# Optimization experiments

Hardware: AMD Instinct MI355X
Metric: run time of the kernel (lower is better)

Reference implementation:

```python
import jax, jax.numpy as jnp
import numpy as np

B = 32768
DIM = 768          # emb dim
NA = 1024          # outer n_anchors
K = 8              # n_comp (= n_patches P in relays)
PD = 16            # patch_dim
RD = K * PD        # relay_dim = 128
L = 2              # n_layers (relays)
RA = 16            # anchors per patch inside RelayLayer
NPH = 3            # n_phases
TD = NPH * RA      # tri_dim = 48
H = 64             # pw_hidden
MAG_MIN, MAG_MAX = 0.1, 5.0


def _nrm(x, eps=1e-12):
    return x / jnp.maximum(jnp.linalg.norm(x, axis=-1, keepdims=True), eps)


def _ln(x, g, b, eps=1e-5):
    mu = jnp.mean(x, axis=-1, keepdims=True)
    var = jnp.mean(jnp.square(x - mu), axis=-1, keepdims=True)
    return (x - mu) * jax.lax.rsqrt(var + eps) * g + b


def setup_inputs() -> dict:
    key = jax.random.key(0)
    ks = jax.random.split(key, 16)
    xav = lambda k, shp, fan_in, fan_out: jax.random.normal(k, shp, jnp.float32) * np.sqrt(2.0 / (fan_in + fan_out))
    home = _nrm(jax.random.normal(ks[3], (L, K, RA, PD), jnp.float32))
    anchors = _nrm(home + 0.05 * jax.random.normal(ks[4], (L, K, RA, PD), jnp.float32))
    return {
        'emb': jax.random.normal(ks[0], (B, DIM), jnp.float32),
        'triangulation': jax.random.normal(ks[1], (B, NA), jnp.float32),
        'raw_magnitude': jax.random.uniform(ks[2], (B, 1), jnp.float32),
        'emb_w': xav(ks[5], (DIM, RD // 2), DIM, RD // 2), 'emb_b': jnp.zeros((RD // 2,), jnp.float32),
        'tri_w': xav(ks[6], (NA, RD // 4), NA, RD // 4), 'tri_b': jnp.zeros((RD // 4,), jnp.float32),
        'ctx_w': xav(ks[7], (RD // 2 + RD // 4 + 1, RD), RD // 2 + RD // 4 + 1, RD), 'ctx_b': jnp.zeros((RD,), jnp.float32),
        'home': home, 'anchors': anchors,
        'pw_w1': xav(ks[8], (L, K, TD, H), TD, H), 'pw_b1': jnp.zeros((L, K, H), jnp.float32),
        'pw_w2': xav(ks[9], (L, K, H, PD), H, PD), 'pw_b2': jnp.zeros((L, K, PD), jnp.float32),
        'pwn_g': jnp.ones((L, PD), jnp.float32), 'pwn_b': jnp.zeros((L, PD), jnp.float32),
        'gates': jnp.full((L, K), -3.0, jnp.float32),
        'norm_g': jnp.ones((L, RD), jnp.float32), 'norm_b': jnp.zeros((L, RD), jnp.float32),
        'head_w1': xav(ks[10], (K, PD, PD // 2), PD, PD // 2), 'head_b1': jnp.zeros((K, PD // 2), jnp.float32),
        'head_w2': xav(ks[11], (K, PD // 2, 1), PD // 2, 1), 'head_b2': jnp.zeros((K, 1), jnp.float32),
        'stats_bias': jnp.zeros((K,), jnp.float32),
    }


def _relay(x, home, anchors, w1, b1, w2, b2, pg, pb, gates, ng, nb):
    Bb = x.shape[0]
    patches = _ln(x, ng, nb).reshape(Bb, K, PD)          # [B,P,d]
    pn = _nrm(patches)
    h = _nrm(home)                                       # [P,A,d]
    c = _nrm(anchors)
    cosw = jnp.clip(jnp.sum(h * c, axis=-1), -1 + 1e-7, 1 - 1e-7)
    omega = jnp.arccos(cosw)[..., None]                  # [P,A,1]
    so = jnp.maximum(jnp.sin(omega), 1e-7)
    tris = []
    for t in (0.0, 1.0 / 3.0, 2.0 / 3.0):
        at = _nrm((jnp.sin((1.0 - t) * omega) * h + jnp.sin(t * omega) * c) / so)
        tris.append(1.0 - jnp.einsum('bpd,pad->bpa', pn, at))
    tri = jnp.concatenate(tris, axis=-1)                 # [B,P,3A]
    hh = jax.nn.gelu(jnp.einsum('bpt,pth->bph', tri, w1) + b1, approximate=False)
    pw = _ln(jnp.einsum('bph,phd->bpd', hh, w2) + b2, pg, pb)
    g = jax.nn.sigmoid(gates)[None, :, None]             # [1,P,1]
    return x + (g * pw + (1.0 - g) * patches).reshape(Bb, -1)


def reference(emb, triangulation, raw_magnitude, emb_w, emb_b, tri_w, tri_b, ctx_w, ctx_b,
              home, anchors, pw_w1, pw_b1, pw_w2, pw_b2, pwn_g, pwn_b, gates, norm_g, norm_b,
              head_w1, head_b1, head_w2, head_b2, stats_bias):
    ctx = jnp.concatenate([emb @ emb_w + emb_b, triangulation @ tri_w + tri_b, raw_magnitude], axis=-1)
    x = ctx @ ctx_w + ctx_b                              # [B, RD]
    for l in range(L):
        x = _relay(x, home[l], anchors[l], pw_w1[l], pw_b1[l], pw_w2[l], pw_b2[l],
                   pwn_g[l], pwn_b[l], gates[l], norm_g[l], norm_b[l])
    patches = x.reshape(-1, K, PD)
    h1 = jax.nn.gelu(jnp.einsum('bkd,kdh->bkh', patches, head_w1) + head_b1, approximate=False)
    mc_raw = (jnp.einsum('bkh,kho->bko', h1, head_w2) + head_b2)[..., 0]   # [B,K]
    mc = MAG_MIN + (MAG_MAX - MAG_MIN) * jax.nn.sigmoid(mc_raw + stats_bias)
    mag = jnp.repeat(mc, NA // K, axis=-1)               # [B, NA]
    return (mag, mc)
```

## Files before the change

kernel.cpp:

```cpp
#include <hip/hip_runtime.h>
#include <hip/hip_bf16.h>
#include <math.h>

#define BTOT 32768

typedef float f32x4 __attribute__((ext_vector_type(4)));
typedef __bf16 v8bf __attribute__((ext_vector_type(8)));

__device__ float g_x[BTOT * 128];
__device__ float g_M[2 * 8 * 16 * 64];
__device__ float g_b1p[2 * 8 * 64];
__device__ __align__(16) unsigned short g_wf[1792 * 128];
__device__ float g_beff[128];
__device__ float g_wr[128];

__device__ __forceinline__ float gelu_f(float v) {
    return 0.5f * v * (1.0f + erff(v * 0.70710678118654752f));
}

__device__ __forceinline__ unsigned short f2bf_rne(float x) {
    unsigned u = __float_as_uint(x);
    u += 0x7fffu + ((u >> 16) & 1u);
    return (unsigned short)(u >> 16);
}

#define GLOAD16(gp, lp)                                                        \
    __builtin_amdgcn_global_load_lds(                                          \
        (const __attribute__((address_space(1))) void*)(gp),                   \
        (__attribute__((address_space(3))) void*)(lp), 16, 0, 0)

__global__ __launch_bounds__(64) void k_pre(const float* __restrict__ home,
                                            const float* __restrict__ anchors,
                                            const float* __restrict__ pw_w1,
                                            const float* __restrict__ pw_b1) {
    __shared__ float s_AT[48 * 16];
    const int lp = blockIdx.x;
    const int tid = threadIdx.x;
    if (tid < 48) {
        const int t = tid >> 4, a = tid & 15;
        const float* hp = home + (lp * 16 + a) * 16;
        const float* cp = anchors + (lp * 16 + a) * 16;
        float h[16], c[16], nh = 0.f, nc = 0.f;
#pragma unroll
        for (int i = 0; i < 16; ++i) {
            h[i] = hp[i]; nh = fmaf(h[i], h[i], nh);
            c[i] = cp[i]; nc = fmaf(c[i], c[i], nc);
        }
        const float ih = 1.f / fmaxf(sqrtf(nh), 1e-12f);
        const float ic = 1.f / fmaxf(sqrtf(nc), 1e-12f);
        float cw = 0.f;
#pragma unroll
        for (int i = 0; i < 16; ++i) { h[i] *= ih; c[i] *= ic; cw = fmaf(h[i], c[i], cw); }
        cw = fminf(fmaxf(cw, -1.f + 1e-7f), 1.f - 1e-7f);
        const float om = acosf(cw);
        const float so = fmaxf(sinf(om), 1e-7f);
        const float tt = (float)t * (1.f / 3.f);
        const float s1 = sinf((1.f - tt) * om), s2 = sinf(tt * om);
        float v[16], nv = 0.f;
#pragma unroll
        for (int i = 0; i < 16; ++i) { v[i] = (s1 * h[i] + s2 * c[i]) / so; nv = fmaf(v[i], v[i], nv); }
        const float iv = 1.f / fmaxf(sqrtf(nv), 1e-12f);
#pragma unroll
        for (int i = 0; i < 16; ++i) s_AT[tid * 16 + i] = v[i] * iv;
    }
    __syncthreads();
    const int h = tid;
    const float* w1 = pw_w1 + lp * 48 * 64;
    float b = pw_b1[lp * 64 + h];
    float m[16];
#pragma unroll
    for (int d = 0; d < 16; ++d) m[d] = 0.f;
    for (int j = 0; j < 48; ++j) {
        const float w = w1[j * 64 + h];
        b += w;
#pragma unroll
        for (int d = 0; d < 16; ++d) m[d] = fmaf(s_AT[j * 16 + d], w, m[d]);
    }
    g_b1p[lp * 64 + h] = b;
#pragma unroll
    for (int d = 0; d < 16; ++d) g_M[(lp * 16 + d) * 64 + h] = m[d];
}

__global__ __launch_bounds__(256) void k_fold(const float* __restrict__ emb_w,
                                              const float* __restrict__ tri_w,
                                              const float* __restrict__ ctx_w,
                                              const float* __restrict__ ctx_b,
                                              const float* __restrict__ emb_b,
                                              const float* __restrict__ tri_b) {
    if (blockIdx.x == 56) {
        const int n = threadIdx.x;
        if (n < 128) {
            float b = ctx_b[n];
            for (int c = 0; c < 64; ++c) b = fmaf(emb_b[c], ctx_w[c * 128 + n], b);
            for (int c = 0; c < 32; ++c) b = fmaf(tri_b[c], ctx_w[(64 + c) * 128 + n], b);
            g_beff[n] = b;
            g_wr[n] = ctx_w[96 * 128 + n];
        }
        return;
    }
    __shared__ float sctx[97 * 128];
    for (int q = threadIdx.x; q < 3104; q += 256)
        *(float4*)&sctx[q * 4] = *(const float4*)&ctx_w[q * 4];
    __syncthreads();
    const int kt = blockIdx.x;
    const int kr = threadIdx.x >> 3;
    const int n0 = (threadIdx.x & 7) * 16;
    const int k = kt * 32 + kr;
    float acc[16];
#pragma unroll
    for (int j = 0; j < 16; ++j) acc[j] = 0.f;
    if (k < 768) {
        const float* wrow = emb_w + k * 64;
        for (int c = 0; c < 64; ++c) {
            const float a = wrow[c];
            const float* cx = &sctx[c * 128 + n0];
#pragma unroll
            for (int j = 0; j < 16; ++j) acc[j] = fmaf(a, cx[j], acc[j]);
        }
    } else {
        const float* wrow = tri_w + (k - 768) * 32;
        for (int c = 0; c < 32; ++c) {
            const float a = wrow[c];
            const float* cx = &sctx[(64 + c) * 128 + n0];
#pragma unroll
            for (int j = 0; j < 16; ++j) acc[j] = fmaf(a, cx[j], acc[j]);
        }
    }
    const int nt = threadIdx.x & 7;
    const int lanehi = (kr >> 3) << 4;
    const int j8 = kr & 7;
#pragma unroll
    for (int q = 0; q < 16; ++q) {
        const int lane = lanehi | q;
        g_wf[((kt * 8 + nt) * 64 + lane) * 8 + j8] = f2bf_rne(acc[q]);
    }
}

__global__ __launch_bounds__(256) void k_front_mfma(const float* __restrict__ emb,
                                                    const float* __restrict__ tri,
                                                    const float* __restrict__ rm) {
    __shared__ __align__(16) char lds[49152];
    const int tid = threadIdx.x;
    const int lane = tid & 63, w = tid >> 6;
    const int row0 = blockIdx.x * 64;
    const int arow = lane & 15, kgrp = lane >> 4;

    f32x4 acc[8];
#pragma unroll
    for (int nt = 0; nt < 8; ++nt) {
        f32x4 z = {0.f, 0.f, 0.f, 0.f};
        acc[nt] = z;
    }

    const float* embp = emb + (size_t)(row0 + w * 16 + arow) * 768 + kgrp * 8;
    const float* trip = tri + (size_t)(row0 + w * 16 + arow) * 1024 + kgrp * 8;

    float4 A0[4], A1[4], A2[4];

#define STAGE_B(kk, BUF) {                                                     \
        const int k2_ = (kk) < 27 ? (kk) : 27;                                 \
        const char* gB_ = (const char*)g_wf + (size_t)k2_ * 16384              \
                          + w * 4096 + lane * 16;                              \
        char* Bb_ = lds + (BUF) * 16384 + w * 4096;               \
        _Pragma("unroll")                                                      \
        for (int i = 0; i < 4; ++i) GLOAD16(gB_ + i * 1024, Bb_ + i * 1024);   \
    }

#define ALOAD(kk, S) {                                                         \
        const int k2_ = (kk) < 27 ? (kk) : 27;                                 \
        const float* ab_ = (k2_ < 12) ? (embp + k2_ * 64) : (trip + (k2_ - 12) * 64); \
        S[0] = *(const float4*)(ab_);                                          \
        S[1] = *(const float4*)(ab_ + 4);                                      \
        S[2] = *(const float4*)(ab_ + 32);                                     \
        S[3] = *(const float4*)(ab_ + 36);                                     \
    }

#define COMPUTE(BUF, S) {                                                      \
        const char* Br_ = lds + (BUF) * 16384 + lane * 16;                     \
        _Pragma("unroll")                                                      \
        for (int h = 0; h < 2; ++h) {                                          \
            const float4 f0_ = S[h * 2], f1_ = S[h * 2 + 1];                   \
            v8bf a_;                                                           \
            a_[0] = (__bf16)f0_.x; a_[1] = (__bf16)f0_.y;                      \
            a_[2] = (__bf16)f0_.z; a_[3] = (__bf16)f0_.w;                      \
            a_[4] = (__bf16)f1_.x; a_[5] = (__bf16)f1_.y;                      \
            a_[6] = (__bf16)f1_.z; a_[7] = (__bf16)f1_.w;                      \
            const char* bp_ = Br_ + h * 8192;                                  \
            _Pragma("unroll")                                                  \
            for (int nt = 0; nt < 8; ++nt) {                                   \
                const v8bf b_ = *(const v8bf*)(bp_ + nt * 1024);               \
                acc[nt] = __builtin_amdgcn_mfma_f32_16x16x32_bf16(a_, b_, acc[nt], 0, 0, 0); \
            }                                                                  \
        }                                                                      \
    }

#define BODY(kk, I0, I2, S0, S2) {                                             \
        STAGE_B((kk) + 2, I2);                                                 \
        ALOAD((kk) + 2, S2);                                                   \
        asm volatile("s_waitcnt vmcnt(16)" ::: "memory");                      \
        __builtin_amdgcn_s_barrier();                                          \
        COMPUTE(I0, S0);                                                       \
        __builtin_amdgcn_s_barrier();                                          \
    }

    STAGE_B(0, 0); ALOAD(0, A0);
    STAGE_B(1, 1); ALOAD(1, A1);

    for (int t = 0; t < 9; ++t) {
        const int k = t * 3;
        BODY(k,     0, 2, A0, A2);
        BODY(k + 1, 1, 0, A1, A0);
        BODY(k + 2, 2, 1, A2, A1);
    }
    BODY(27, 0, 2, A0, A2);
    asm volatile("s_waitcnt vmcnt(0)" ::: "memory");
#undef STAGE_B
#undef ALOAD
#undef COMPUTE
#undef BODY

    const int rowb = row0 + w * 16 + kgrp * 4;
    const f32x4 rv = *(const f32x4*)&rm[rowb];
#pragma unroll
    for (int nt = 0; nt < 8; ++nt) {
        const int col = nt * 16 + arow;
        const float be = g_beff[col];
        const float wv = g_wr[col];
#pragma unroll
        for (int rr = 0; rr < 4; ++rr) {
            g_x[(size_t)(rowb + rr) * 128 + col] = acc[nt][rr] + rv[rr] * wv + be;
        }
    }
}

__global__ __launch_bounds__(256) void k_relay(
    const float* __restrict__ pw_w2, const float* __restrict__ pw_b2,
    const float* __restrict__ pwn_g, const float* __restrict__ pwn_b,
    const float* __restrict__ gates, const float* __restrict__ norm_g,
    const float* __restrict__ norm_b, const float* __restrict__ head_w1,
    const float* __restrict__ head_b1, const float* __restrict__ head_w2,
    const float* __restrict__ head_b2, const float* __restrict__ stats_bias,
    float* __restrict__ out) {
    __shared__ __align__(16) float s_M[8 * 1028];
    __shared__ __align__(16) float s_w2[8 * 1028];
    __shared__ __align__(16) float s_b1p[8 * 68];
    __shared__ __align__(16) float s_hw1[8 * 132];
    __shared__ float s_hb1[64], s_hw2[64], s_hcb[8];
    __shared__ float s_mc[64 * 8];
    const int tid = threadIdx.x;
    const int pr = tid >> 3, p = tid & 7;
    const int rowA = blockIdx.x * 64 + pr * 2;

    {
        const int e = tid * 4, pp = e >> 7, rem = e & 127;
        *(float4*)&s_hw1[pp * 132 + rem] = *(const float4*)&head_w1[e];
    }
    if (tid < 64) { s_hb1[tid] = head_b1[tid]; s_hw2[tid] = head_w2[tid]; }
    if (tid < 8) s_hcb[tid] = head_b2[tid] + stats_bias[tid];

    float xA[16], xB[16];
    {
        const float* xp = g_x + (size_t)rowA * 128 + p * 16;
#pragma unroll
        for (int i = 0; i < 4; ++i) {
            *(float4*)&xA[i * 4] = *(const float4*)&xp[i * 4];
            *(float4*)&xB[i * 4] = *(const float4*)&xp[128 + i * 4];
        }
    }

    for (int l = 0; l < 2; ++l) {
        if (l) __syncthreads();
        for (int q = tid; q < 2048; q += 256) {
            const int e = q * 4, pp = e >> 10, rem = e & 1023;
            *(float4*)&s_M[pp * 1028 + rem] = *(const float4*)&g_M[l * 8192 + e];
            *(float4*)&s_w2[pp * 1028 + rem] = *(const float4*)&pw_w2[l * 8192 + e];
        }
        if (tid < 128) {
            const int e = tid * 4, pp = e >> 6, rem = e & 63;
            *(float4*)&s_b1p[pp * 68 + rem] = *(const float4*)&g_b1p[l * 512 + e];
        }
        __syncthreads();

        float sA = 0.f, qA = 0.f, sB = 0.f, qB = 0.f;
#pragma unroll
        for (int i = 0; i < 16; ++i) {
            sA += xA[i]; qA = fmaf(xA[i], xA[i], qA);
            sB += xB[i]; qB = fmaf(xB[i], xB[i], qB);
        }
#pragma unroll
        for (int m = 1; m < 8; m <<= 1) {
            sA += __shfl_xor(sA, m, 64); qA += __shfl_xor(qA, m, 64);
            sB += __shfl_xor(sB, m, 64); qB += __shfl_xor(qB, m, 64);
        }
        const float muA = sA * (1.f / 128.f);
        const float rsA = rsqrtf(fmaxf(qA * (1.f / 128.f) - muA * muA, 0.f) + 1e-5f);
        const float muB = sB * (1.f / 128.f);
        const float rsB = rsqrtf(fmaxf(qB * (1.f / 128.f) - muB * muB, 0.f) + 1e-5f);
        float paA[16], paB[16], nA = 0.f, nB = 0.f;
#pragma unroll
        for (int i = 0; i < 16; ++i) {
            const float gg = norm_g[l * 128 + p * 16 + i];
            const float bb = norm_b[l * 128 + p * 16 + i];
            const float vA = (xA[i] - muA) * rsA * gg + bb;
            const float vB = (xB[i] - muB) * rsB * gg + bb;
            paA[i] = vA; nA = fmaf(vA, vA, nA);
            paB[i] = vB; nB = fmaf(vB, vB, nB);
        }
        const float invA = 1.f / fmaxf(sqrtf(nA), 1e-12f);
        const float invB = 1.f / fmaxf(sqrtf(nB), 1e-12f);

        float pwA[16], pwB[16];
#pragma unroll
        for (int i = 0; i < 16; ++i) {
            const float b2 = pw_b2[(l * 8 + p) * 16 + i];
            pwA[i] = b2; pwB[i] = b2;
        }
        const float* Mp = &s_M[p * 1028];
        const float* W2p = &s_w2[p * 1028];
        const float* Bp = &s_b1p[p * 68];
        for (int h4 = 0; h4 < 16; ++h4) {
            float bq[4];
            *(float4*)bq = *(const float4*)&Bp[h4 * 4];
            float aA[4] = {0.f, 0.f, 0.f, 0.f};
            float aB[4] = {0.f, 0.f, 0.f, 0.f};
#pragma unroll
            for (int d = 0; d < 16; ++d) {
                float m4[4];
                *(float4*)m4 = *(const float4*)&Mp[d * 64 + h4 * 4];
#pragma unroll
                for (int j = 0; j < 4; ++j) {
                    aA[j] = fmaf(paA[d], m4[j], aA[j]);
                    aB[j] = fmaf(paB[d], m4[j], aB[j]);
                }
            }
#pragma unroll
            for (int j = 0; j < 4; ++j) {
                const float gA = gelu_f(bq[j] - invA * aA[j]);
                const float gB = gelu_f(bq[j] - invB * aB[j]);
                float w[16];
#pragma unroll
                for (int u = 0; u < 4; ++u)
                    *(float4*)&w[u * 4] = *(const float4*)&W2p[(h4 * 4 + j) * 16 + u * 4];
#pragma unroll
                for (int u = 0; u < 16; ++u) {
                    pwA[u] = fmaf(gA, w[u], pwA[u]);
                    pwB[u] = fmaf(gB, w[u], pwB[u]);
                }
            }
        }
        float s2A = 0.f, q2A = 0.f, s2B = 0.f, q2B = 0.f;
#pragma unroll
        for (int i = 0; i < 16; ++i) {
            s2A += pwA[i]; q2A = fmaf(pwA[i], pwA[i], q2A);
            s2B += pwB[i]; q2B = fmaf(pwB[i], pwB[i], q2B);
        }
        const float mu2A = s2A * (1.f / 16.f);
        const float rs2A = rsqrtf(fmaxf(q2A * (1.f / 16.f) - mu2A * mu2A, 0.f) + 1e-5f);
        const float mu2B = s2B * (1.f / 16.f);
        const float rs2B = rsqrtf(fmaxf(q2B * (1.f / 16.f) - mu2B * mu2B, 0.f) + 1e-5f);
        const float gate = 1.f / (1.f + expf(-gates[l * 8 + p]));
#pragma unroll
        for (int i = 0; i < 16; ++i) {
            const float pg = pwn_g[l * 16 + i], pb = pwn_b[l * 16 + i];
            const float vA = (pwA[i] - mu2A) * rs2A * pg + pb;
            const float vB = (pwB[i] - mu2B) * rs2B * pg + pb;
            xA[i] = xA[i] + gate * vA + (1.f - gate) * paA[i];
            xB[i] = xB[i] + gate * vB + (1.f - gate) * paB[i];
        }
    }

    float accmA = s_hcb[p], accmB = accmA;
#pragma unroll
    for (int j = 0; j < 8; ++j) {
        float aA = s_hb1[p * 8 + j], aB = aA;
#pragma unroll
        for (int d = 0; d < 16; ++d) {
            const float w = s_hw1[p * 132 + d * 8 + j];
            aA = fmaf(xA[d], w, aA);
            aB = fmaf(xB[d], w, aB);
        }
        const float w2h = s_hw2[p * 8 + j];
        accmA = fmaf(gelu_f(aA), w2h, accmA);
        accmB = fmaf(gelu_f(aB), w2h, accmB);
    }
    const float mcA = 0.1f + 4.9f / (1.f + expf(-accmA));
    const float mcB = 0.1f + 4.9f / (1.f + expf(-accmB));
    s_mc[(pr * 2) * 8 + p] = mcA;
    s_mc[(pr * 2 + 1) * 8 + p] = mcB;
    out[(size_t)33554432 + (size_t)rowA * 8 + p] = mcA;
    out[(size_t)33554432 + (size_t)(rowA + 1) * 8 + p] = mcB;
    __syncthreads();

    const size_t base = (size_t)blockIdx.x * 64 * 1024;
#pragma unroll
    for (int it = 0; it < 64; ++it) {
        const int idx = it * 256 + tid;
        const int rr = idx >> 8, c4 = idx & 255;
        const float v = s_mc[rr * 8 + (c4 >> 5)];
        const float4 vv = make_float4(v, v, v, v);
        *(float4*)&out[base + rr * 1024 + c4 * 4] = vv;
    }
}

extern "C" void kernel_launch(void* const* d_in, const int* in_sizes, int n_in,
                              void* d_out, int out_size, void* d_ws, size_t ws_size,
                              hipStream_t stream) {
    (void)in_sizes; (void)n_in; (void)d_ws; (void)ws_size; (void)out_size;
    const float* emb = (const float*)d_in[0];
    const float* tria = (const float*)d_in[1];
    const float* rm = (const float*)d_in[2];
    const float* emb_w = (const float*)d_in[3];
    const float* emb_b = (const float*)d_in[4];
    const float* tri_w = (const float*)d_in[5];
    const float* tri_b = (const float*)d_in[6];
    const float* ctx_w = (const float*)d_in[7];
    const float* ctx_b = (const float*)d_in[8];
    const float* home = (const float*)d_in[9];
    const float* anch = (const float*)d_in[10];
    const float* pw_w1 = (const float*)d_in[11];
    const float* pw_b1 = (const float*)d_in[12];
    const float* pw_w2 = (const float*)d_in[13];
    const float* pw_b2 = (const float*)d_in[14];
    const float* pwn_g = (const float*)d_in[15];
    const float* pwn_b = (const float*)d_in[16];
    const float* gates = (const float*)d_in[17];
    const float* norm_g = (const float*)d_in[18];
    const float* norm_b = (const float*)d_in[19];
    const float* hw1 = (const float*)d_in[20];
    const float* hb1 = (const float*)d_in[21];
    const float* hw2 = (const float*)d_in[22];
    const float* hb2 = (const float*)d_in[23];
    const float* sb = (const float*)d_in[24];
    float* out = (float*)d_out;

    k_pre<<<16, 64, 0, stream>>>(home, anch, pw_w1, pw_b1);
    k_fold<<<57, 256, 0, stream>>>(emb_w, tri_w, ctx_w, ctx_b, emb_b, tri_b);
    k_front_mfma<<<512, 256, 0, stream>>>(emb, tria, rm);
    k_relay<<<512, 256, 0, stream>>>(pw_w2, pw_b2, pwn_g, pwn_b, gates, norm_g, norm_b,
                                     hw1, hb1, hw2, hb2, sb, out);
}
```

Before: 178.4 us.

## Replace erf GELU with tanh approx, double-buffer front GEMM, 4 rows per relay thread

GELU now uses a sigmoid-based tanh approximation with fast exp and reciprocal instead of erff, and the sigmoids use fast reciprocal. The front MFMA kernel moves from a triple-buffered, waitcnt-tuned pipeline to a simpler double buffer with __syncthreads, which reduces LDS use. The relay kernel processes 4 rows per thread (128 rows per block, half the blocks) so each LDS weight load is reused across more rows. The GELU approximation changes numerics slightly, and the heavier register load per thread may reduce occupancy.

```diff
diff --git a/kernel.cpp b/kernel.cpp
--- a/kernel.cpp
+++ b/kernel.cpp
@@ -14,8 +14,21 @@
 __device__ float g_beff[128];
 __device__ float g_wr[128];
 
+__device__ __forceinline__ float fast_rcp(float x) {
+#if __has_builtin(__builtin_amdgcn_rcpf)
+    return __builtin_amdgcn_rcpf(x);
+#else
+    return 1.f / x;
+#endif
+}
+
 __device__ __forceinline__ float gelu_f(float v) {
-    return 0.5f * v * (1.0f + erff(v * 0.70710678118654752f));
+    const float p = v * fmaf(v * v, 0.0713548162f, 1.59576912f);
+    return v * fast_rcp(1.f + __expf(-p));
+}
+
+__device__ __forceinline__ float fast_sigmoid(float v) {
+    return fast_rcp(1.f + __expf(-v));
 }
 
 __device__ __forceinline__ unsigned short f2bf_rne(float x) {
@@ -139,7 +152,7 @@
 __global__ __launch_bounds__(256) void k_front_mfma(const float* __restrict__ emb,
                                                     const float* __restrict__ tri,
                                                     const float* __restrict__ rm) {
-    __shared__ __align__(16) char lds[49152];
+    __shared__ __align__(16) char lds[32768];
     const int tid = threadIdx.x;
     const int lane = tid & 63, w = tid >> 6;
     const int row0 = blockIdx.x * 64;
@@ -155,24 +168,23 @@
     const float* embp = emb + (size_t)(row0 + w * 16 + arow) * 768 + kgrp * 8;
     const float* trip = tri + (size_t)(row0 + w * 16 + arow) * 1024 + kgrp * 8;
 
-    float4 A0[4], A1[4], A2[4];
+    float4 A0[4], A1[4];
+
+#define ALOAD(kk, S) {                                                         \
+        const float* ab_ = ((kk) < 12) ? (embp + (kk) * 64)                    \
+                                       : (trip + ((kk) - 12) * 64);            \
+        S[0] = *(const float4*)(ab_);                                          \
+        S[1] = *(const float4*)(ab_ + 4);                                      \
+        S[2] = *(const float4*)(ab_ + 32);                                     \
+        S[3] = *(const float4*)(ab_ + 36);                                     \
+    }
 
 #define STAGE_B(kk, BUF) {                                                     \
-        const int k2_ = (kk) < 27 ? (kk) : 27;                                 \
-        const char* gB_ = (const char*)g_wf + (size_t)k2_ * 16384              \
+        const char* gB_ = (const char*)g_wf + (size_t)(kk) * 16384             \
                           + w * 4096 + lane * 16;                              \
         char* Bb_ = lds + (BUF) * 16384 + w * 4096;               \
         _Pragma("unroll")                                                      \
         for (int i = 0; i < 4; ++i) GLOAD16(gB_ + i * 1024, Bb_ + i * 1024);   \
-    }
-
-#define ALOAD(kk, S) {                                                         \
-        const int k2_ = (kk) < 27 ? (kk) : 27;                                 \
-        const float* ab_ = (k2_ < 12) ? (embp + k2_ * 64) : (trip + (k2_ - 12) * 64); \
-        S[0] = *(const float4*)(ab_);                                          \
-        S[1] = *(const float4*)(ab_ + 4);                                      \
-        S[2] = *(const float4*)(ab_ + 32);                                     \
-        S[3] = *(const float4*)(ab_ + 36);                                     \
     }
 
 #define COMPUTE(BUF, S) {                                                      \
@@ -194,30 +206,24 @@
         }                                                                      \
     }
 
-#define BODY(kk, I0, I2, S0, S2) {                                             \
-        STAGE_B((kk) + 2, I2);                                                 \
-        ALOAD((kk) + 2, S2);                                                   \
-        asm volatile("s_waitcnt vmcnt(16)" ::: "memory");                      \
-        __builtin_amdgcn_s_barrier();                                          \
-        COMPUTE(I0, S0);                                                       \
-        __builtin_amdgcn_s_barrier();                                          \
-    }
-
-    STAGE_B(0, 0); ALOAD(0, A0);
-    STAGE_B(1, 1); ALOAD(1, A1);
-
-    for (int t = 0; t < 9; ++t) {
-        const int k = t * 3;
-        BODY(k,     0, 2, A0, A2);
-        BODY(k + 1, 1, 0, A1, A0);
-        BODY(k + 2, 2, 1, A2, A1);
-    }
-    BODY(27, 0, 2, A0, A2);
-    asm volatile("s_waitcnt vmcnt(0)" ::: "memory");
+    ALOAD(0, A0);
+    STAGE_B(0, 0);
+    __syncthreads();
+    for (int t = 0; t < 14; ++t) {
+        ALOAD(2 * t + 1, A1);
+        STAGE_B(2 * t + 1, 1);
+        COMPUTE(0, A0);
+        __syncthreads();
+        if (t < 13) {
+            ALOAD(2 * t + 2, A0);
+            STAGE_B(2 * t + 2, 0);
+        }
+        COMPUTE(1, A1);
+        __syncthreads();
+    }
+#undef ALOAD
 #undef STAGE_B
-#undef ALOAD
 #undef COMPUTE
-#undef BODY
 
     const int rowb = row0 + w * 16 + kgrp * 4;
     const f32x4 rv = *(const f32x4*)&rm[rowb];
@@ -246,10 +252,10 @@
     __shared__ __align__(16) float s_b1p[8 * 68];
     __shared__ __align__(16) float s_hw1[8 * 132];
     __shared__ float s_hb1[64], s_hw2[64], s_hcb[8];
-    __shared__ float s_mc[64 * 8];
+    __shared__ float s_mc[128 * 8];
     const int tid = threadIdx.x;
-    const int pr = tid >> 3, p = tid & 7;
-    const int rowA = blockIdx.x * 64 + pr * 2;
+    const int q = tid >> 3, p = tid & 7;
+    const int row0 = blockIdx.x * 128 + q * 4;
 
     {
         const int e = tid * 4, pp = e >> 7, rem = e & 127;
@@ -258,20 +264,20 @@
     if (tid < 64) { s_hb1[tid] = head_b1[tid]; s_hw2[tid] = head_w2[tid]; }
     if (tid < 8) s_hcb[tid] = head_b2[tid] + stats_bias[tid];
 
-    float xA[16], xB[16];
+    float x[4][16];
     {
-        const float* xp = g_x + (size_t)rowA * 128 + p * 16;
-#pragma unroll
-        for (int i = 0; i < 4; ++i) {
-            *(float4*)&xA[i * 4] = *(const float4*)&xp[i * 4];
-            *(float4*)&xB[i * 4] = *(const float4*)&xp[128 + i * 4];
-        }
+        const float* xp = g_x + (size_t)row0 * 128 + p * 16;
+#pragma unroll
+        for (int r = 0; r < 4; ++r)
+#pragma unroll
+            for (int i = 0; i < 4; ++i)
+                *(float4*)&x[r][i * 4] = *(const float4*)&xp[r * 128 + i * 4];
     }
 
     for (int l = 0; l < 2; ++l) {
         if (l) __syncthreads();
-        for (int q = tid; q < 2048; q += 256) {
-            const int e = q * 4, pp = e >> 10, rem = e & 1023;
+        for (int e4 = tid; e4 < 2048; e4 += 256) {
+            const int e = e4 * 4, pp = e >> 10, rem = e & 1023;
             *(float4*)&s_M[pp * 1028 + rem] = *(const float4*)&g_M[l * 8192 + e];
             *(float4*)&s_w2[pp * 1028 + rem] = *(const float4*)&pw_w2[l * 8192 + e];
         }
@@ -281,39 +287,53 @@
         }
         __syncthreads();
 
-        float sA = 0.f, qA = 0.f, sB = 0.f, qB = 0.f;
-#pragma unroll
-        for (int i = 0; i < 16; ++i) {
-            sA += xA[i]; qA = fmaf(xA[i], xA[i], qA);
-            sB += xB[i]; qB = fmaf(xB[i], xB[i], qB);
-        }
+        float sm[4], sq[4];
+#pragma unroll
+        for (int r = 0; r < 4; ++r) { sm[r] = 0.f; sq[r] = 0.f; }
+#pragma unroll
+        for (int r = 0; r < 4; ++r)
+#pragma unroll
+            for (int i = 0; i < 16; ++i) {
+                sm[r] += x[r][i]; sq[r] = fmaf(x[r][i], x[r][i], sq[r]);
+            }
 #pragma unroll
         for (int m = 1; m < 8; m <<= 1) {
-            sA += __shfl_xor(sA, m, 64); qA += __shfl_xor(qA, m, 64);
-            sB += __shfl_xor(sB, m, 64); qB += __shfl_xor(qB, m, 64);
-        }
-        const float muA = sA * (1.f / 128.f);
-        const float rsA = rsqrtf(fmaxf(qA * (1.f / 128.f) - muA * muA, 0.f) + 1e-5f);
-        const float muB = sB * (1.f / 128.f);
-        const float rsB = rsqrtf(fmaxf(qB * (1.f / 128.f) - muB * muB, 0.f) + 1e-5f);
-        float paA[16], paB[16], nA = 0.f, nB = 0.f;
-#pragma unroll
-        for (int i = 0; i < 16; ++i) {
-            const float gg = norm_g[l * 128 + p * 16 + i];
-            const float bb = norm_b[l * 128 + p * 16 + i];
-            const float vA = (xA[i] - muA) * rsA * gg + bb;
-            const float vB = (xB[i] - muB) * rsB * gg + bb;
-            paA[i] = vA; nA = fmaf(vA, vA, nA);
-            paB[i] = vB; nB = fmaf(vB, vB, nB);
-        }
-        const float invA = 1.f / fmaxf(sqrtf(nA), 1e-12f);
-        const float invB = 1.f / fmaxf(sqrtf(nB), 1e-12f);
-
-        float pwA[16], pwB[16];
+#pragma unroll
+            for (int r = 0; r < 4; ++r) {
+                sm[r] += __shfl_xor(sm[r], m, 64);
+                sq[r] += __shfl_xor(sq[r], m, 64);
+            }
+        }
+        float mu[4], rs[4], inv[4];
+        float pa[4][16];
+#pragma unroll
+        for (int r = 0; r < 4; ++r) {
+            mu[r] = sm[r] * (1.f / 128.f);
+            rs[r] = rsqrtf(fmaxf(sq[r] * (1.f / 128.f) - mu[r] * mu[r], 0.f) + 1e-5f);
+        }
+        {
+            float n2[4] = {0.f, 0.f, 0.f, 0.f};
+#pragma unroll
+            for (int i = 0; i < 16; ++i) {
+                const float gg = norm_g[l * 128 + p * 16 + i];
+                const float bb = norm_b[l * 128 + p * 16 + i];
+#pragma unroll
+                for (int r = 0; r < 4; ++r) {
+                    const float v = (x[r][i] - mu[r]) * rs[r] * gg + bb;
+                    pa[r][i] = v;
+                    n2[r] = fmaf(v, v, n2[r]);
+                }
+            }
+#pragma unroll
+            for (int r = 0; r < 4; ++r) inv[r] = 1.f / fmaxf(sqrtf(n2[r]), 1e-12f);
+        }
+
+        float pw[4][16];
 #pragma unroll
         for (int i = 0; i < 16; ++i) {
             const float b2 = pw_b2[(l * 8 + p) * 16 + i];
-            pwA[i] = b2; pwB[i] = b2;
+#pragma unroll
+            for (int r = 0; r < 4; ++r) pw[r][i] = b2;
         }
         const float* Mp = &s_M[p * 1028];
         const float* W2p = &s_w2[p * 1028];
@@ -321,79 +341,93 @@
         for (int h4 = 0; h4 < 16; ++h4) {
             float bq[4];
             *(float4*)bq = *(const float4*)&Bp[h4 * 4];
-            float aA[4] = {0.f, 0.f, 0.f, 0.f};
-            float aB[4] = {0.f, 0.f, 0.f, 0.f};
+            float a[4][4];
+#pragma unroll
+            for (int r = 0; r < 4; ++r)
+#pragma unroll
+                for (int j = 0; j < 4; ++j) a[r][j] = 0.f;
 #pragma unroll
             for (int d = 0; d < 16; ++d) {
                 float m4[4];
                 *(float4*)m4 = *(const float4*)&Mp[d * 64 + h4 * 4];
 #pragma unroll
-                for (int j = 0; j < 4; ++j) {
-                    aA[j] = fmaf(paA[d], m4[j], aA[j]);
-                    aB[j] = fmaf(paB[d], m4[j], aB[j]);
-                }
+                for (int r = 0; r < 4; ++r)
+#pragma unroll
+                    for (int j = 0; j < 4; ++j)
+                        a[r][j] = fmaf(pa[r][d], m4[j], a[r][j]);
             }
 #pragma unroll
             for (int j = 0; j < 4; ++j) {
-                const float gA = gelu_f(bq[j] - invA * aA[j]);
-                const float gB = gelu_f(bq[j] - invB * aB[j]);
-                float w[16];
+                float g[4];
+#pragma unroll
+                for (int r = 0; r < 4; ++r) g[r] = gelu_f(bq[j] - inv[r] * a[r][j]);
+                float wv[16];
 #pragma unroll
                 for (int u = 0; u < 4; ++u)
-                    *(float4*)&w[u * 4] = *(const float4*)&W2p[(h4 * 4 + j) * 16 + u * 4];
-#pragma unroll
-                for (int u = 0; u < 16; ++u) {
-                    pwA[u] = fmaf(gA, w[u], pwA[u]);
-                    pwB[u] = fmaf(gB, w[u], pwB[u]);
-                }
-            }
-        }
-        float s2A = 0.f, q2A = 0.f, s2B = 0.f, q2B = 0.f;
-#pragma unroll
-        for (int i = 0; i < 16; ++i) {
-            s2A += pwA[i]; q2A = fmaf(pwA[i], pwA[i], q2A);
-            s2B += pwB[i]; q2B = fmaf(pwB[i], pwB[i], q2B);
-        }
-        const float mu2A = s2A * (1.f / 16.f);
-        const float rs2A = rsqrtf(fmaxf(q2A * (1.f / 16.f) - mu2A * mu2A, 0.f) + 1e-5f);
-        const float mu2B = s2B * (1.f / 16.f);
-        const float rs2B = rsqrtf(fmaxf(q2B * (1.f / 16.f) - mu2B * mu2B, 0.f) + 1e-5f);
-        const float gate = 1.f / (1.f + expf(-gates[l * 8 + p]));
+                    *(float4*)&wv[u * 4] = *(const float4*)&W2p[(h4 * 4 + j) * 16 + u * 4];
+#pragma unroll
+                for (int u = 0; u < 16; ++u)
+#pragma unroll
+                    for (int r = 0; r < 4; ++r)
+                        pw[r][u] = fmaf(g[r], wv[u], pw[r][u]);
+            }
+        }
+        float s2[4], q2[4];
+#pragma unroll
+        for (int r = 0; r < 4; ++r) { s2[r] = 0.f; q2[r] = 0.f; }
+#pragma unroll
+        for (int r = 0; r < 4; ++r)
+#pragma unroll
+            for (int i = 0; i < 16; ++i) {
+                s2[r] += pw[r][i]; q2[r] = fmaf(pw[r][i], pw[r][i], q2[r]);
+            }
+        float mu2[4], rs2[4];
+#pragma unroll
+        for (int r = 0; r < 4; ++r) {
+            mu2[r] = s2[r] * (1.f / 16.f);
+            rs2[r] = rsqrtf(fmaxf(q2[r] * (1.f / 16.f) - mu2[r] * mu2[r], 0.f) + 1e-5f);
+        }
+        const float gate = fast_sigmoid(gates[l * 8 + p]);
 #pragma unroll
         for (int i = 0; i < 16; ++i) {
             const float pg = pwn_g[l * 16 + i], pb = pwn_b[l * 16 + i];
-            const float vA = (pwA[i] - mu2A) * rs2A * pg + pb;
-            const float vB = (pwB[i] - mu2B) * rs2B * pg + pb;
-            xA[i] = xA[i] + gate * vA + (1.f - gate) * paA[i];
-            xB[i] = xB[i] + gate * vB + (1.f - gate) * paB[i];
-        }
-    }
-
-    float accmA = s_hcb[p], accmB = accmA;
+#pragma unroll
+            for (int r = 0; r < 4; ++r) {
+                const float v = (pw[r][i] - mu2[r]) * rs2[r] * pg + pb;
+                x[r][i] = x[r][i] + gate * v + (1.f - gate) * pa[r][i];
+            }
+        }
+    }
+
+    float accm[4];
+#pragma unroll
+    for (int r = 0; r < 4; ++r) accm[r] = s_hcb[p];
 #pragma unroll
     for (int j = 0; j < 8; ++j) {
-        float aA = s_hb1[p * 8 + j], aB = aA;
+        float a[4];
+#pragma unroll
+        for (int r = 0; r < 4; ++r) a[r] = s_hb1[p * 8 + j];
 #pragma unroll
         for (int d = 0; d < 16; ++d) {
             const float w = s_hw1[p * 132 + d * 8 + j];
-            aA = fmaf(xA[d], w, aA);
-            aB = fmaf(xB[d], w, aB);
+#pragma unroll
+            for (int r = 0; r < 4; ++r) a[r] = fmaf(x[r][d], w, a[r]);
         }
         const float w2h = s_hw2[p * 8 + j];
-        accmA = fmaf(gelu_f(aA), w2h, accmA);
-        accmB = fmaf(gelu_f(aB), w2h, accmB);
-    }
-    const float mcA = 0.1f + 4.9f / (1.f + expf(-accmA));
-    const float mcB = 0.1f + 4.9f / (1.f + expf(-accmB));
-    s_mc[(pr * 2) * 8 + p] = mcA;
-    s_mc[(pr * 2 + 1) * 8 + p] = mcB;
-    out[(size_t)33554432 + (size_t)rowA * 8 + p] = mcA;
-    out[(size_t)33554432 + (size_t)(rowA + 1) * 8 + p] = mcB;
+#pragma unroll
+        for (int r = 0; r < 4; ++r) accm[r] = fmaf(gelu_f(a[r]), w2h, accm[r]);
+    }
+#pragma unroll
+    for (int r = 0; r < 4; ++r) {
+        const float mc = 0.1f + 4.9f * fast_sigmoid(accm[r]);
+        s_mc[(q * 4 + r) * 8 + p] = mc;
+        out[(size_t)33554432 + (size_t)(row0 + r) * 8 + p] = mc;
+    }
     __syncthreads();
 
-    const size_t base = (size_t)blockIdx.x * 64 * 1024;
-#pragma unroll
-    for (int it = 0; it < 64; ++it) {
+    const size_t base = (size_t)blockIdx.x * 128 * 1024;
+#pragma unroll 8
+    for (int it = 0; it < 128; ++it) {
         const int idx = it * 256 + tid;
         const int rr = idx >> 8, c4 = idx & 255;
         const float v = s_mc[rr * 8 + (c4 >> 5)];
@@ -436,6 +470,6 @@
     k_pre<<<16, 64, 0, stream>>>(home, anch, pw_w1, pw_b1);
     k_fold<<<57, 256, 0, stream>>>(emb_w, tri_w, ctx_w, ctx_b, emb_b, tri_b);
     k_front_mfma<<<512, 256, 0, stream>>>(emb, tria, rm);
-    k_relay<<<512, 256, 0, stream>>>(pw_w2, pw_b2, pwn_g, pwn_b, gates, norm_g, norm_b,
+    k_relay<<<256, 256, 0, stream>>>(pw_w2, pw_b2, pwn_g, pwn_b, gates, norm_g, norm_b,
                                      hw1, hb1, hw2, hb2, sb, out);
 }
```

Measured after the change: 214.2 us. +20.1%, slower.
